# Optimization experiments

Measured on AMD Instinct MI355X. Metric: run time of the kernel, lower is better.

Reference implementation:

```python
import jax, jax.numpy as jnp
import numpy as np

NUM_ROUTES, NUM_TIME, DIM, K, C = 100000, 2016, 256, 100, 5
BATCH = 262144


def _xavier(key, shape):
    fan_in, fan_out = shape[0], shape[1]
    lim = np.sqrt(6.0 / (fan_in + fan_out))
    return jax.random.uniform(key, shape, jnp.float32, -lim, lim)


def setup_inputs() -> dict:
    key = jax.random.key(0)
    ks = jax.random.split(key, 9)
    route_idx = jax.random.randint(ks[0], (BATCH,), 0, NUM_ROUTES)
    time_idx = jax.random.randint(ks[1], (BATCH,), 0, NUM_TIME)
    route_table = _xavier(ks[2], (NUM_ROUTES, DIM))
    time_table = _xavier(ks[3], (NUM_TIME, DIM))
    w = _xavier(ks[4], (DIM, K))
    mode_a = _xavier(ks[5], (DIM, C))
    mode_b = _xavier(ks[6], (DIM, C))
    mode_bias = jnp.zeros((C, C), jnp.float32)
    fc_lim = 1.0 / np.sqrt(C * C + K)
    fc_w = jax.random.uniform(ks[7], (C * C + K, 1), jnp.float32, -fc_lim, fc_lim)
    fc_b = jax.random.uniform(ks[8], (1,), jnp.float32, -fc_lim, fc_lim)
    return {
        "route_idx": route_idx, "time_idx": time_idx,
        "route_table": route_table, "time_table": time_table,
        "w": w, "mode_a": mode_a, "mode_b": mode_b,
        "mode_bias": mode_bias, "fc_w": fc_w, "fc_b": fc_b,
    }


def reference(route_idx, time_idx, route_table, time_table, w, mode_a, mode_b, mode_bias, fc_w, fc_b):
    r = route_table[route_idx]            # [B, D]
    t = time_table[time_idx]              # [B, D]
    gcp = jax.nn.relu((r * t) @ w)        # [B, K]
    # einsum('ni,nj->nij') then contracting i with mode_a and j with mode_b
    # equals outer product of the two small projections (exact same math):
    ra = r @ mode_a                       # [B, C]
    tb = t @ mode_b                       # [B, C]
    inter = jax.nn.sigmoid(ra[:, :, None] * tb[:, None, :] + mode_bias)  # [B, C, C]
    feats = jnp.concatenate([gcp, inter.reshape(inter.shape[0], -1)], axis=1)  # [B, K + C*C]
    out = feats @ fc_w + fc_b             # [B, 1]
    return jnp.squeeze(out, axis=-1)      # [B]
```

## Files before the change

kernel.cpp:

```cpp
#include <hip/hip_runtime.h>
#include <stdint.h>

#define BATCH   262144
#define NROUTES 100000
#define NTIME   2016
#define DIM     256
#define KOUT    100
#define NTILES  7

typedef __attribute__((ext_vector_type(2))) float f32x2;
typedef __attribute__((ext_vector_type(4))) float f32x4;

#define WS_WFRAG_BYTES ((size_t)(NTILES * 8 * 64 * 8))
#define WS_RA_OFF   (WS_WFRAG_BYTES)
#define WS_TB_OFF   (WS_RA_OFF + (size_t)NROUTES * 32)
#define WS_RT8_OFF  (WS_TB_OFF + (size_t)NTIME * 32)
#define WS_TT8_OFF  (WS_RT8_OFF + (size_t)NROUTES * 256)
#define WS_NEED     (WS_TT8_OFF + (size_t)NTIME * 256)

template<int CTRL>
static __device__ __forceinline__ float dpp_add(float x) {
  int s = __builtin_amdgcn_update_dpp(0, __builtin_bit_cast(int, x), CTRL, 0xF, 0xF, true);
  return x + __builtin_bit_cast(float, s);
}
static __device__ __forceinline__ float wave_sum63(float x) {
  x = dpp_add<0x111>(x);
  x = dpp_add<0x112>(x);
  x = dpp_add<0x114>(x);
  x = dpp_add<0x118>(x);
  x = dpp_add<0x142>(x);
  x = dpp_add<0x143>(x);
  return x;
}
static __device__ __forceinline__ float sum16_all(float x) {
  x = dpp_add<0x0B1>(x);
  x = dpp_add<0x04E>(x);
  x = dpp_add<0x124>(x);
  x = dpp_add<0x128>(x);
  return x;
}

__global__ __launch_bounds__(256) void prep_kernel(
    const float* __restrict__ route_table,
    const float* __restrict__ time_table,
    const float* __restrict__ w,
    const float* __restrict__ mode_a,
    const float* __restrict__ mode_b,
    uint8_t* __restrict__ ws, int do8)
{
  const int b   = blockIdx.x;
  const int tid = threadIdx.x;

  if (b < 14) {
    const int u = b * 256 + tid;
    const int lane = u & 63;
    const int frag = u >> 6;
    const int ks = frag / NTILES;
    const int nt = frag % NTILES;
    const int n  = nt * 16 + (lane & 15);
    const int k0 = ks * 32 + (lane >> 4) * 8;
    float v[8];
    #pragma unroll
    for (int j = 0; j < 8; ++j)
      v[j] = (n < KOUT) ? w[(size_t)(k0 + j) * KOUT + n] : 0.0f;
    uint32_t d0 = 0, d1 = 0;
    d0 = __builtin_amdgcn_cvt_pk_fp8_f32(v[0], v[1], d0, false);
    d0 = __builtin_amdgcn_cvt_pk_fp8_f32(v[2], v[3], d0, true);
    d1 = __builtin_amdgcn_cvt_pk_fp8_f32(v[4], v[5], d1, false);
    d1 = __builtin_amdgcn_cvt_pk_fp8_f32(v[6], v[7], d1, true);
    ((uint2*)ws)[u] = make_uint2(d0, d1);
    return;
  }

  const float* tab; const float* proj; float* outp; uint8_t* out8; int base;
  if (b < 14 + 126) {
    tab = time_table;  proj = mode_b; outp = (float*)(ws + WS_TB_OFF);
    out8 = ws + WS_TT8_OFF; base = (b - 14) * 16;
  } else {
    tab = route_table; proj = mode_a; outp = (float*)(ws + WS_RA_OFF);
    out8 = ws + WS_RT8_OFF; base = (b - 140) * 16;
  }

  const int wave = tid >> 6, lane = tid & 63;
  float A[4][5];
  #pragma unroll
  for (int j = 0; j < 4; ++j)
    #pragma unroll
    for (int i = 0; i < 5; ++i)
      A[j][i] = proj[(4 * lane + j) * 5 + i];

  const int p0 = (lane >> 4) * 64 + ((lane >> 1) & 3) * 16 +
                 ((lane >> 3) & 1) * 8 + (lane & 1) * 4;

  const int row0 = base + wave * 4;
  float4 v[4];
  #pragma unroll
  for (int rr = 0; rr < 4; ++rr)
    v[rr] = *(const float4*)(tab + (size_t)(row0 + rr) * DIM + 4 * lane);

  #pragma unroll
  for (int rr = 0; rr < 4; ++rr) {
    const int row = row0 + rr;
    if (do8) {
      uint32_t u = 0;
      u = __builtin_amdgcn_cvt_pk_fp8_f32(8.f * v[rr].x, 8.f * v[rr].y, u, false);
      u = __builtin_amdgcn_cvt_pk_fp8_f32(8.f * v[rr].z, 8.f * v[rr].w, u, true);
      *(uint32_t*)(out8 + (size_t)row * 256 + p0) = u;
    }
    float p[5];
    #pragma unroll
    for (int i = 0; i < 5; ++i) {
      float s = v[rr].x * A[0][i] + v[rr].y * A[1][i] + v[rr].z * A[2][i] + v[rr].w * A[3][i];
      p[i] = wave_sum63(s);
    }
    if (lane == 63) {
      float* o = outp + (size_t)row * 8;
      *(f32x4*)o = (f32x4){p[0], p[1], p[2], p[3]};
      o[4] = p[4];
    }
  }
}

template<int TAB8>
__global__ __launch_bounds__(256, 4) void main_kernel(
    const int*   __restrict__ route_idx,
    const int*   __restrict__ time_idx,
    const float* __restrict__ route_table,
    const float* __restrict__ time_table,
    const float* __restrict__ mode_bias,
    const float* __restrict__ fc_w,
    const float* __restrict__ fc_b,
    const uint8_t* __restrict__ ws,
    float* __restrict__ out)
{
  const int tid  = threadIdx.x;
  const int wave = tid >> 6, lane = tid & 63;
  const int col  = lane & 15, quad = lane >> 4;
  const int m0   = blockIdx.x * 64 + wave * 16;
  const size_t ri = (size_t)route_idx[m0 + col];
  const size_t ti = (size_t)time_idx[m0 + col];
  const bool desig = (quad == (col >> 2));

  f32x4 ra0; float ra4; f32x4 tb0; float tb4;
  if (desig) {
    const float* ra = (const float*)(ws + WS_RA_OFF) + ri * 8;
    const float* tb = (const float*)(ws + WS_TB_OFF) + ti * 8;
    ra0 = *(const f32x4*)ra; ra4 = ra[4];
    tb0 = *(const f32x4*)tb; tb4 = tb[4];
  }

  uint4 rw[4], tw[4];
  if (TAB8) {
    const uint8_t* rb = ws + WS_RT8_OFF + ri * 256 + quad * 16;
    const uint8_t* tb = ws + WS_TT8_OFF + ti * 256 + quad * 16;
    #pragma unroll
    for (int i = 0; i < 4; ++i) {
      rw[i] = *(const uint4*)(rb + i * 64);
      tw[i] = *(const uint4*)(tb + i * 64);
    }
  }

  float fcw_l[NTILES];
  #pragma unroll
  for (int nt = 0; nt < NTILES; ++nt) {
    const int n = nt * 16 + col;
    fcw_l[nt] = (n < KOUT) ? fc_w[n] * 0.015625f : 0.0f;
  }

  f32x4 acc[NTILES];
  #pragma unroll
  for (int nt = 0; nt < NTILES; ++nt) acc[nt] = (f32x4){0.f, 0.f, 0.f, 0.f};
  const uint2* wfr = (const uint2*)ws;

  #pragma unroll
  for (int ks = 0; ks < 8; ++ks) {
    uint32_t p0, p1;
    if (TAB8) {
      const int i = ks >> 1;
      const uint32_t ra = (ks & 1) ? rw[i].z : rw[i].x;
      const uint32_t rb = (ks & 1) ? rw[i].w : rw[i].y;
      const uint32_t ta = (ks & 1) ? tw[i].z : tw[i].x;
      const uint32_t tb = (ks & 1) ? tw[i].w : tw[i].y;
      f32x2 r01 = __builtin_amdgcn_cvt_pk_f32_fp8(ra, false);
      f32x2 r23 = __builtin_amdgcn_cvt_pk_f32_fp8(ra, true);
      f32x2 r45 = __builtin_amdgcn_cvt_pk_f32_fp8(rb, false);
      f32x2 r67 = __builtin_amdgcn_cvt_pk_f32_fp8(rb, true);
      f32x2 t01 = __builtin_amdgcn_cvt_pk_f32_fp8(ta, false);
      f32x2 t23 = __builtin_amdgcn_cvt_pk_f32_fp8(ta, true);
      f32x2 t45 = __builtin_amdgcn_cvt_pk_f32_fp8(tb, false);
      f32x2 t67 = __builtin_amdgcn_cvt_pk_f32_fp8(tb, true);
      f32x2 x01 = r01 * t01, x23 = r23 * t23, x45 = r45 * t45, x67 = r67 * t67;
      p0 = 0; p1 = 0;
      p0 = __builtin_amdgcn_cvt_pk_fp8_f32(x01.x, x01.y, p0, false);
      p0 = __builtin_amdgcn_cvt_pk_fp8_f32(x23.x, x23.y, p0, true);
      p1 = __builtin_amdgcn_cvt_pk_fp8_f32(x45.x, x45.y, p1, false);
      p1 = __builtin_amdgcn_cvt_pk_fp8_f32(x67.x, x67.y, p1, true);
    } else {
      const float4* rp = (const float4*)(route_table + ri * DIM + ks * 32 + quad * 8);
      const float4* tp = (const float4*)(time_table  + ti * DIM + ks * 32 + quad * 8);
      float4 r0 = rp[0], r1 = rp[1], t0 = tp[0], t1 = tp[1];
      p0 = 0; p1 = 0;
      p0 = __builtin_amdgcn_cvt_pk_fp8_f32(64.f * r0.x * t0.x, 64.f * r0.y * t0.y, p0, false);
      p0 = __builtin_amdgcn_cvt_pk_fp8_f32(64.f * r0.z * t0.z, 64.f * r0.w * t0.w, p0, true);
      p1 = __builtin_amdgcn_cvt_pk_fp8_f32(64.f * r1.x * t1.x, 64.f * r1.y * t1.y, p1, false);
      p1 = __builtin_amdgcn_cvt_pk_fp8_f32(64.f * r1.z * t1.z, 64.f * r1.w * t1.w, p1, true);
    }
    const long a64 = __builtin_bit_cast(long, make_uint2(p0, p1));
    #pragma unroll
    for (int nt = 0; nt < NTILES; ++nt) {
      const long b64 = __builtin_bit_cast(long, wfr[(ks * NTILES + nt) * 64 + lane]);
      acc[nt] = __builtin_amdgcn_mfma_f32_16x16x32_fp8_fp8(a64, b64, acc[nt], 0, 0, 0);
    }
  }

  float s[4];
  #pragma unroll
  for (int reg = 0; reg < 4; ++reg) {
    float v = 0.f;
    #pragma unroll
    for (int nt = 0; nt < NTILES; ++nt)
      v += fmaxf(acc[nt][reg], 0.f) * fcw_l[nt];
    s[reg] = sum16_all(v);
  }

  if (desig) {
    const int m = col;
    const float sa = (m & 1) ? s[1] : s[0];
    const float sb = (m & 1) ? s[3] : s[2];
    float o = fc_b[0] + ((m & 2) ? sb : sa);
    const float rav[5] = {ra0.x, ra0.y, ra0.z, ra0.w, ra4};
    const float tbv[5] = {tb0.x, tb0.y, tb0.z, tb0.w, tb4};
    #pragma unroll
    for (int i = 0; i < 5; ++i)
      #pragma unroll
      for (int j = 0; j < 5; ++j) {
        const float z  = rav[i] * tbv[j] + mode_bias[i * 5 + j];
        const float sg = 1.0f / (1.0f + __expf(-z));
        o += sg * fc_w[KOUT + i * 5 + j];
      }
    out[m0 + m] = o;
  }
}

extern "C" void kernel_launch(void* const* d_in, const int* in_sizes, int n_in,
                              void* d_out, int out_size, void* d_ws, size_t ws_size,
                              hipStream_t stream)
{
  const int*   route_idx   = (const int*)d_in[0];
  const int*   time_idx    = (const int*)d_in[1];
  const float* route_table = (const float*)d_in[2];
  const float* time_table  = (const float*)d_in[3];
  const float* w           = (const float*)d_in[4];
  const float* mode_a      = (const float*)d_in[5];
  const float* mode_b      = (const float*)d_in[6];
  const float* mode_bias   = (const float*)d_in[7];
  const float* fc_w        = (const float*)d_in[8];
  const float* fc_b        = (const float*)d_in[9];
  uint8_t* ws  = (uint8_t*)d_ws;
  float*   out = (float*)d_out;

  const int big = (ws_size >= WS_NEED) ? 1 : 0;

  prep_kernel<<<6390, 256, 0, stream>>>(route_table, time_table, w,
                                        mode_a, mode_b, ws, big);
  if (big)
    main_kernel<1><<<BATCH / 64, 256, 0, stream>>>(route_idx, time_idx,
                                                   route_table, time_table,
                                                   mode_bias, fc_w, fc_b, ws, out);
  else
    main_kernel<0><<<BATCH / 64, 256, 0, stream>>>(route_idx, time_idx,
                                                   route_table, time_table,
                                                   mode_bias, fc_w, fc_b, ws, out);
}
```

Baseline: 225.5 us.

## Stage W fragments in LDS and spread sigmoid interaction work across quads

Each block now copies the 28 KB of pre-packed fp8 weight fragments from global memory into shared memory once, with a barrier, and the MFMA loop reads B operands from LDS instead of global/L2. The 25-term sigmoid interaction is split across the four quad lanes per row (about 6-7 sigmoids each, using a hardware reciprocal) and combined with cross-lane shuffles, replacing 25 serial sigmoids on one designated lane. This trades a per-block LDS fill and sync, plus 28 KB of LDS per block that may limit occupancy, for fewer global loads and better lane utilization in the epilogue.

```diff
diff --git a/kernel.cpp b/kernel.cpp
--- a/kernel.cpp
+++ b/kernel.cpp
@@ -38,6 +38,9 @@
   x = dpp_add<0x124>(x);
   x = dpp_add<0x128>(x);
   return x;
+}
+static __device__ __forceinline__ float sigm(float z) {
+  return __builtin_amdgcn_rcpf(1.0f + __expf(-z));
 }
 
 __global__ __launch_bounds__(256) void prep_kernel(
@@ -133,21 +136,13 @@
     const uint8_t* __restrict__ ws,
     float* __restrict__ out)
 {
+  __shared__ uint4 wlds[1792];
   const int tid  = threadIdx.x;
   const int wave = tid >> 6, lane = tid & 63;
   const int col  = lane & 15, quad = lane >> 4;
   const int m0   = blockIdx.x * 64 + wave * 16;
   const size_t ri = (size_t)route_idx[m0 + col];
   const size_t ti = (size_t)time_idx[m0 + col];
-  const bool desig = (quad == (col >> 2));
-
-  f32x4 ra0; float ra4; f32x4 tb0; float tb4;
-  if (desig) {
-    const float* ra = (const float*)(ws + WS_RA_OFF) + ri * 8;
-    const float* tb = (const float*)(ws + WS_TB_OFF) + ti * 8;
-    ra0 = *(const f32x4*)ra; ra4 = ra[4];
-    tb0 = *(const f32x4*)tb; tb4 = tb[4];
-  }
 
   uint4 rw[4], tw[4];
   if (TAB8) {
@@ -159,6 +154,18 @@
       tw[i] = *(const uint4*)(tb + i * 64);
     }
   }
+  const float* rap = (const float*)(ws + WS_RA_OFF) + ri * 8;
+  const float* tbp = (const float*)(ws + WS_TB_OFF) + ti * 8;
+  f32x4 ra0 = *(const f32x4*)rap; float ra4 = rap[4];
+  f32x4 tb0 = *(const f32x4*)tbp; float tb4 = tbp[4];
+
+  {
+    const uint4* wsrc = (const uint4*)ws;
+    #pragma unroll
+    for (int j = 0; j < 7; ++j)
+      wlds[j * 256 + tid] = wsrc[j * 256 + tid];
+  }
+  __syncthreads();
 
   float fcw_l[NTILES];
   #pragma unroll
@@ -170,7 +177,7 @@
   f32x4 acc[NTILES];
   #pragma unroll
   for (int nt = 0; nt < NTILES; ++nt) acc[nt] = (f32x4){0.f, 0.f, 0.f, 0.f};
-  const uint2* wfr = (const uint2*)ws;
+  const uint2* wl2 = (const uint2*)wlds;
 
   #pragma unroll
   for (int ks = 0; ks < 8; ++ks) {
@@ -208,7 +215,7 @@
     const long a64 = __builtin_bit_cast(long, make_uint2(p0, p1));
     #pragma unroll
     for (int nt = 0; nt < NTILES; ++nt) {
-      const long b64 = __builtin_bit_cast(long, wfr[(ks * NTILES + nt) * 64 + lane]);
+      const long b64 = __builtin_bit_cast(long, wl2[(ks * NTILES + nt) * 64 + lane]);
       acc[nt] = __builtin_amdgcn_mfma_f32_16x16x32_fp8_fp8(a64, b64, acc[nt], 0, 0, 0);
     }
   }
@@ -223,22 +230,27 @@
     s[reg] = sum16_all(v);
   }
 
-  if (desig) {
-    const int m = col;
-    const float sa = (m & 1) ? s[1] : s[0];
-    const float sb = (m & 1) ? s[3] : s[2];
-    float o = fc_b[0] + ((m & 2) ? sb : sa);
-    const float rav[5] = {ra0.x, ra0.y, ra0.z, ra0.w, ra4};
-    const float tbv[5] = {tb0.x, tb0.y, tb0.z, tb0.w, tb4};
-    #pragma unroll
-    for (int i = 0; i < 5; ++i)
-      #pragma unroll
-      for (int j = 0; j < 5; ++j) {
-        const float z  = rav[i] * tbv[j] + mode_bias[i * 5 + j];
-        const float sg = 1.0f / (1.0f + __expf(-z));
-        o += sg * fc_w[KOUT + i * 5 + j];
-      }
-    out[m0 + m] = o;
+  const float rav[5] = {ra0.x, ra0.y, ra0.z, ra0.w, ra4};
+  const float tbv[5] = {tb0.x, tb0.y, tb0.z, tb0.w, tb4};
+  const float rq = (quad & 2) ? ((quad & 1) ? rav[3] : rav[2])
+                              : ((quad & 1) ? rav[1] : rav[0]);
+  const float tq = (quad & 2) ? ((quad & 1) ? tbv[3] : tbv[2])
+                              : ((quad & 1) ? tbv[1] : tbv[0]);
+  float sig = 0.f;
+  #pragma unroll
+  for (int j = 0; j < 5; ++j)
+    sig += sigm(rq * tbv[j] + mode_bias[5 * quad + j]) * fc_w[KOUT + 5 * quad + j];
+  sig += sigm(rav[4] * tq + mode_bias[20 + quad]) * fc_w[KOUT + 20 + quad];
+  if (quad == 0)
+    sig += sigm(rav[4] * tbv[4] + mode_bias[24]) * fc_w[KOUT + 24];
+  sig += __shfl_xor(sig, 16, 64);
+  sig += __shfl_xor(sig, 32, 64);
+
+  if (quad == (col >> 2)) {
+    const float sa = (col & 1) ? s[1] : s[0];
+    const float sb = (col & 1) ? s[3] : s[2];
+    const float gcp = (col & 2) ? sb : sa;
+    out[m0 + col] = fc_b[0] + gcp + sig;
   }
 }
 
```

After: 203.3 us. 1.11x faster.
